# Kernel optimization log

Measured on AMD Instinct MI355X. Metric: run time of the kernel, lower is better.

The kernel has to match this reference:

```python
import jax, jax.numpy as jnp
import numpy as np

NUM_HEADS = 16
D_MODEL = 1024


def setup_inputs() -> dict:
    key = jax.random.key(0)
    ks = jax.random.split(key, 12)
    B, S, D = 2, 2048, D_MODEL
    inp = {
        "query": jax.random.normal(ks[0], (B, S, D), dtype=jnp.float32),
        "key": jax.random.normal(ks[1], (B, S, D), dtype=jnp.float32),
        "value": jax.random.normal(ks[2], (B, S, D), dtype=jnp.float32),
        "mask": jax.random.randint(ks[3], (B, 1, S), 0, 2).astype(jnp.bool_),
    }
    # Linear layer params, stored as (in, out) so y = x @ W + b
    sd = 1.0 / np.sqrt(D)
    for i, nm in enumerate(["q", "k", "v", "o"]):
        inp[f"W{nm}"] = jax.random.uniform(ks[4 + 2 * i], (D, D), jnp.float32, -sd, sd)
        inp[f"b{nm}"] = jax.random.uniform(ks[5 + 2 * i], (D,), jnp.float32, -sd, sd)
    return inp


def _split_heads(x):
    # [B, S, D] -> [B, H, S, d_k]
    B, S, D = x.shape
    return x.reshape(B, S, NUM_HEADS, D // NUM_HEADS).transpose(0, 2, 1, 3)


def reference(query, key, value, mask, Wq, bq, Wk, bk, Wv, bv, Wo, bo):
    B, Sq, D = query.shape
    d_k = D // NUM_HEADS
    scale = 1.0 / np.sqrt(d_k)

    q = _split_heads(query @ Wq + bq)   # [B,H,Sq,dk]
    k = _split_heads(key @ Wk + bk)     # [B,H,Sk,dk]
    v = _split_heads(value @ Wv + bv)   # [B,H,Sk,dk]

    scores = jnp.einsum("bhqd,bhkd->bhqk", q, k) * scale  # [B,H,Sq,Sk]
    # mask: [B,1,Sk] bool, True = masked; broadcast over heads and queries
    scores = jnp.where(mask[:, None, :, :], -jnp.inf, scores)
    attn = jax.nn.softmax(scores, axis=-1)
    attn = jnp.nan_to_num(attn, nan=0.0)  # fully-masked rows -> 0 (matches torch)

    ctx = jnp.einsum("bhqk,bhkd->bhqd", attn, v)  # [B,H,Sq,dk]
    ctx = ctx.transpose(0, 2, 1, 3).reshape(B, Sq, D)  # combine heads
    out = ctx @ Wo + bo
    return out
```

## Files before the change

kernel.cpp:

```cpp
#include <hip/hip_runtime.h>


typedef unsigned short u16;
typedef __attribute__((ext_vector_type(8))) short bf16x8;
typedef __attribute__((ext_vector_type(4))) float f32x4;
typedef __attribute__((ext_vector_type(2))) unsigned int u32x2;

static __device__ __forceinline__ u16 f2bf(float x) {
  union { float f; unsigned int i; } v; v.f = x;
  return (u16)((v.i + 0x8000u) >> 16);
}
static __device__ __forceinline__ float bf2f(u16 u) {
  union { unsigned int i; float f; } v; v.i = ((unsigned int)u) << 16; return v.f;
}

static __device__ __forceinline__ unsigned int cvtpk(float lo, float hi) {
  unsigned int r;
  asm("v_cvt_pk_bf16_f32 %0, %1, %2" : "=v"(r) : "v"(lo), "v"(hi));
  return r;
}

#define MFMA_B16(a, b, c) __builtin_amdgcn_mfma_f32_16x16x32_bf16((a), (b), (c), 0, 0, 0)

__global__ __launch_bounds__(256) void prep_w(
    const float* __restrict__ w0, const float* __restrict__ w1,
    const float* __restrict__ w2, const float* __restrict__ w3,
    u16* __restrict__ t0, u16* __restrict__ t1,
    u16* __restrict__ t2, u16* __restrict__ t3) {
  __shared__ u16 tile[64 * 68];
  const float* W; u16* T;
  switch (blockIdx.z) {
    case 0: W = w0; T = t0; break;
    case 1: W = w1; T = t1; break;
    case 2: W = w2; T = t2; break;
    default: W = w3; T = t3; break;
  }
  const int t = threadIdx.x;
  const int k0 = blockIdx.x * 64, n0 = blockIdx.y * 64;
#pragma unroll
  for (int it = 0; it < 4; ++it) {
    int idx = it * 256 + t;
    int r = idx >> 4, c4 = idx & 15;
    float4 v = *(const float4*)&W[(size_t)(k0 + r) * 1024 + n0 + c4 * 4];
    tile[r * 68 + c4 * 4 + 0] = f2bf(v.x);
    tile[r * 68 + c4 * 4 + 1] = f2bf(v.y);
    tile[r * 68 + c4 * 4 + 2] = f2bf(v.z);
    tile[r * 68 + c4 * 4 + 3] = f2bf(v.w);
  }
  __syncthreads();
#pragma unroll
  for (int it = 0; it < 2; ++it) {
    int idx = it * 256 + t;
    int n = idx >> 3, kc = idx & 7;
    bf16x8 pk;
#pragma unroll
    for (int j = 0; j < 8; ++j) pk[j] = (short)tile[(kc * 8 + j) * 68 + n];
    *(bf16x8*)&T[(size_t)(n0 + n) * 1024 + k0 + kc * 8] = pk;
  }
}

template <int MT, int AMODE, int OMODE>
__global__ __launch_bounds__(256) void gemm_bias(
    const void* a0v, const void* a1v, const void* a2v,
    const u16* __restrict__ Wt,
    const float* b0, const float* b1, const float* b2,
    void* o0, void* o1, void* o2) {
  __shared__ __align__(16) u16 As[MT * 32 * 32];
  __shared__ __align__(16) u16 Bs[128 * 32];
  const int t = threadIdx.x, wave = t >> 6, lane = t & 63;
  const int l15 = lane & 15, quad = lane >> 4;
  const int m0 = blockIdx.x * (MT * 32);
  const int n0 = blockIdx.y * 128;
  const int rg = (OMODE == 3) ? (n0 >> 10) : 0;
  const void* Av = (rg == 0) ? a0v : (rg == 1 ? a1v : a2v);
  const float* bp = (rg == 0) ? b0 : (rg == 1 ? b1 : b2);
  const int nb = (OMODE == 3) ? (n0 & 1023) : n0;
  const int wr = (wave >> 1) * (MT * 16), wc = (wave & 1) * 64;

  const f32x4 fz = {0.f, 0.f, 0.f, 0.f};
  f32x4 acc[MT][4];
#pragma unroll
  for (int mt = 0; mt < MT; ++mt)
#pragma unroll
    for (int nt = 0; nt < 4; ++nt) acc[mt][nt] = fz;

  float4 pa[MT / 2][2]; bf16x8 pab[MT / 2]; bf16x8 pb[2];
#pragma unroll
  for (int s = 0; s < MT / 2; ++s) {
    int idx = s * 256 + t, row = idx >> 2, seg = idx & 3;
    if (AMODE == 1) {
      const float* ap = (const float*)Av + (size_t)(m0 + row) * 1024 + seg * 8;
      pa[s][0] = *(const float4*)ap; pa[s][1] = *(const float4*)(ap + 4);
    } else {
      pab[s] = *(const bf16x8*)((const u16*)Av + (size_t)(m0 + row) * 1024 + seg * 8);
    }
  }
#pragma unroll
  for (int s = 0; s < 2; ++s) {
    int idx = s * 256 + t, row = idx >> 2, seg = idx & 3;
    pb[s] = *(const bf16x8*)&Wt[(size_t)(n0 + row) * 1024 + seg * 8];
  }

  for (int kb = 0; kb < 1024; kb += 32) {
    __syncthreads();
#pragma unroll
    for (int s = 0; s < MT / 2; ++s) {
      int idx = s * 256 + t, row = idx >> 2, seg = idx & 3;
      bf16x8 pk;
      if (AMODE == 1) {
        pk[0] = (short)f2bf(pa[s][0].x); pk[1] = (short)f2bf(pa[s][0].y);
        pk[2] = (short)f2bf(pa[s][0].z); pk[3] = (short)f2bf(pa[s][0].w);
        pk[4] = (short)f2bf(pa[s][1].x); pk[5] = (short)f2bf(pa[s][1].y);
        pk[6] = (short)f2bf(pa[s][1].z); pk[7] = (short)f2bf(pa[s][1].w);
      } else pk = pab[s];
      *(bf16x8*)&As[row * 32 + seg * 8] = pk;
    }
#pragma unroll
    for (int s = 0; s < 2; ++s) {
      int idx = s * 256 + t, row = idx >> 2, seg = idx & 3;
      *(bf16x8*)&Bs[row * 32 + seg * 8] = pb[s];
    }
    __syncthreads();
    const int kn = (kb + 32) & 1023;
#pragma unroll
    for (int s = 0; s < MT / 2; ++s) {
      int idx = s * 256 + t, row = idx >> 2, seg = idx & 3;
      if (AMODE == 1) {
        const float* ap = (const float*)Av + (size_t)(m0 + row) * 1024 + kn + seg * 8;
        pa[s][0] = *(const float4*)ap; pa[s][1] = *(const float4*)(ap + 4);
      } else {
        pab[s] = *(const bf16x8*)((const u16*)Av + (size_t)(m0 + row) * 1024 + kn + seg * 8);
      }
    }
#pragma unroll
    for (int s = 0; s < 2; ++s) {
      int idx = s * 256 + t, row = idx >> 2, seg = idx & 3;
      pb[s] = *(const bf16x8*)&Wt[(size_t)(n0 + row) * 1024 + kn + seg * 8];
    }
    bf16x8 a[MT], bfr[4];
#pragma unroll
    for (int mt = 0; mt < MT; ++mt)
      a[mt] = *(const bf16x8*)&As[(wr + mt * 16 + l15) * 32 + quad * 8];
#pragma unroll
    for (int nt = 0; nt < 4; ++nt)
      bfr[nt] = *(const bf16x8*)&Bs[(wc + nt * 16 + l15) * 32 + quad * 8];
#pragma unroll
    for (int mt = 0; mt < MT; ++mt)
#pragma unroll
      for (int nt = 0; nt < 4; ++nt)
        acc[mt][nt] = MFMA_B16(a[mt], bfr[nt], acc[mt][nt]);
  }

#pragma unroll
  for (int nt = 0; nt < 4; ++nt) {
    const int n = nb + wc + nt * 16 + l15;
    const float bv = bp[n];
#pragma unroll
    for (int mt = 0; mt < MT; ++mt)
#pragma unroll
      for (int r = 0; r < 4; ++r) {
        const int m = m0 + wr + mt * 16 + quad * 4 + r;
        const float val = acc[mt][nt][r] + bv;
        if (OMODE == 2) {
          ((float*)o0)[(size_t)m * 1024 + n] = val;
        } else if (OMODE == 0) {
          ((u16*)o0)[(size_t)m * 1024 + n] = f2bf(val);
        } else {
          if (rg == 0)      ((u16*)o0)[(size_t)m * 1024 + n] = f2bf(val);
          else if (rg == 1) ((u16*)o1)[(size_t)m * 1024 + n] = f2bf(val);
          else {
            const int h = n >> 6, d = n & 63, bb = m >> 11, ss = m & 2047;
            ((u16*)o2)[((size_t)(bb * 16 + h) * 64 + d) * 2048 + ss] = f2bf(val);
          }
        }
      }
  }
}

__global__ __launch_bounds__(512) void attn_fused(
    const u16* Q, const u16* __restrict__ K,
    const u16* __restrict__ Vt, const int* __restrict__ mask,
    u16* ctx) {
  __shared__ __align__(16) u16 Ks[128 * 72];
  __shared__ __align__(16) u16 Vs[64 * 136];
  __shared__ __align__(16) u16 Pl[8][16 * 136];
  __shared__ __align__(16) float Mf[2048];
  const int t = threadIdx.x, wave = t >> 6, lane = t & 63;
  const int l15 = lane & 15, quad = lane >> 4;
  const int bh = blockIdx.y, b = bh >> 4, h = bh & 15;
  const int q0 = blockIdx.x * 128 + wave * 16;
  const float cs = 0.125f * 1.44269504f;

#pragma unroll
  for (int i = 0; i < 4; ++i) {
    int idx = i * 512 + t;
    Mf[idx] = mask[b * 2048 + idx] ? -__builtin_inff() : 0.f;
  }

  const u16* Qp = Q + (size_t)(b * 2048 + q0) * 1024 + h * 64;
  const bf16x8 qf0 = *(const bf16x8*)(Qp + (size_t)l15 * 1024 + quad * 8);
  const bf16x8 qf1 = *(const bf16x8*)(Qp + (size_t)l15 * 1024 + 32 + quad * 8);

  const u16* Kbase = K + (size_t)(b * 2048) * 1024 + h * 64;
  const u16* Vbase = Vt + (size_t)bh * 64 * 2048;

  const int kr0 = t >> 3,        kc0 = (t & 7) * 8;
  const int kr1 = (512 + t) >> 3;
  const int vr0 = t >> 4,        vc0 = (t & 15) * 8;
  const int vr1 = (512 + t) >> 4;

  bf16x8 gk0 = *(const bf16x8*)&Kbase[(size_t)kr0 * 1024 + kc0];
  bf16x8 gk1 = *(const bf16x8*)&Kbase[(size_t)kr1 * 1024 + kc0];
  bf16x8 gv0 = *(const bf16x8*)&Vbase[(size_t)vr0 * 2048 + vc0];
  bf16x8 gv1 = *(const bf16x8*)&Vbase[(size_t)vr1 * 2048 + vc0];

  const f32x4 fz = {0.f, 0.f, 0.f, 0.f};
  f32x4 o[4];
  float lsum = 0.f;
#pragma unroll
  for (int i = 0; i < 4; ++i) o[i] = fz;

  for (int kt = 0; kt < 2048; kt += 128) {
    __syncthreads();
    *(bf16x8*)&Ks[kr0 * 72 + kc0] = gk0;
    *(bf16x8*)&Ks[kr1 * 72 + kc0] = gk1;
    *(bf16x8*)&Vs[vr0 * 136 + vc0] = gv0;
    *(bf16x8*)&Vs[vr1 * 136 + vc0] = gv1;
    __syncthreads();
    const int kn = (kt + 128) & 2047;
    gk0 = *(const bf16x8*)&Kbase[(size_t)(kn + kr0) * 1024 + kc0];
    gk1 = *(const bf16x8*)&Kbase[(size_t)(kn + kr1) * 1024 + kc0];
    gv0 = *(const bf16x8*)&Vbase[(size_t)vr0 * 2048 + kn + vc0];
    gv1 = *(const bf16x8*)&Vbase[(size_t)vr1 * 2048 + kn + vc0];

#pragma unroll
    for (int nt = 0; nt < 8; ++nt) {
      const int krow = nt * 16 + l15;
      bf16x8 k0 = *(const bf16x8*)&Ks[krow * 72 + quad * 8];
      bf16x8 k1 = *(const bf16x8*)&Ks[krow * 72 + 32 + quad * 8];
      f32x4 acc = MFMA_B16(k0, qf0, fz);
      acc = MFMA_B16(k1, qf1, acc);
      const float4 bias4 = *(const float4*)&Mf[kt + nt * 16 + quad * 4];
      float p0 = exp2f(fmaf(acc[0], cs, bias4.x));
      float p1 = exp2f(fmaf(acc[1], cs, bias4.y));
      float p2 = exp2f(fmaf(acc[2], cs, bias4.z));
      float p3 = exp2f(fmaf(acc[3], cs, bias4.w));
      lsum += (p0 + p1) + (p2 + p3);
      u32x2 pp;
      pp.x = cvtpk(p0, p1);
      pp.y = cvtpk(p2, p3);
      *(u32x2*)&Pl[wave][l15 * 136 + nt * 16 + quad * 4] = pp;
    }
#pragma unroll
    for (int kc = 0; kc < 4; ++kc) {
      const bf16x8 pf = *(const bf16x8*)&Pl[wave][l15 * 136 + kc * 32 + quad * 8];
#pragma unroll
      for (int nt = 0; nt < 4; ++nt) {
        const bf16x8 vf = *(const bf16x8*)&Vs[(nt * 16 + l15) * 136 + kc * 32 + quad * 8];
        o[nt] = MFMA_B16(pf, vf, o[nt]);
      }
    }
  }
  lsum += __shfl_xor(lsum, 16);
  lsum += __shfl_xor(lsum, 32);
  u16* cp = ctx + (size_t)(b * 2048 + q0) * 1024 + h * 64;
#pragma unroll
  for (int r = 0; r < 4; ++r) {
    const float lrow = __shfl(lsum, quad * 4 + r);
    const bool ok = lrow > 0.f;
    const float inv = ok ? 1.f / lrow : 0.f;
#pragma unroll
    for (int nt = 0; nt < 4; ++nt)
      cp[(quad * 4 + r) * 1024 + nt * 16 + l15] = f2bf(ok ? o[nt][r] * inv : 0.f);
  }
}

extern "C" void kernel_launch(void* const* d_in, const int* in_sizes, int n_in,
                              void* d_out, int out_size, void* d_ws, size_t ws_size,
                              hipStream_t stream) {
  const float* q    = (const float*)d_in[0];
  const float* k    = (const float*)d_in[1];
  const float* v    = (const float*)d_in[2];
  const int*   mask = (const int*)d_in[3];
  const float* Wq = (const float*)d_in[4];  const float* bq = (const float*)d_in[5];
  const float* Wk = (const float*)d_in[6];  const float* bk = (const float*)d_in[7];
  const float* Wv = (const float*)d_in[8];  const float* bv = (const float*)d_in[9];
  const float* Wo = (const float*)d_in[10]; const float* bo = (const float*)d_in[11];

  char* ws = (char*)d_ws;
  u16*   Kp  = (u16*)(ws + ((size_t)0 << 20));
  u16*   Vt  = (u16*)(ws + ((size_t)8 << 20));
  float* O32 = (float*)ws;

  char* od = (char*)d_out;
  u16* ctx = (u16*)od;
  u16* WqT = (u16*)(od + ((size_t)8 << 20));
  u16* WkT = (u16*)(od + ((size_t)10 << 20));
  u16* WvT = (u16*)(od + ((size_t)12 << 20));
  u16* WoT = (u16*)(od + ((size_t)14 << 20));

  dim3 blk(256);
  prep_w<<<dim3(16, 16, 4), blk, 0, stream>>>(Wq, Wk, Wv, Wo, WqT, WkT, WvT, WoT);
  gemm_bias<4, 1, 3><<<dim3(32, 24), blk, 0, stream>>>(
      q, k, v, WqT, bq, bk, bv, (void*)ctx, (void*)Kp, (void*)Vt);
  attn_fused<<<dim3(16, 32), dim3(512), 0, stream>>>(ctx, Kp, Vt, mask, ctx);
  gemm_bias<2, 0, 2><<<dim3(64, 8), blk, 0, stream>>>(
      ctx, nullptr, nullptr, WoT, bo, nullptr, nullptr, (void*)O32, nullptr, nullptr);
  hipMemcpyAsync(d_out, O32, (size_t)out_size * sizeof(float),
                 hipMemcpyDeviceToDevice, stream);
}
```

Baseline: 263.8 us.

## Swizzle attention LDS tiles, shrink P buffer and stream mask per tile

Replaces padded LDS layouts for K, V and the per-wave P tile with XOR-swizzled unpadded layouts. The P tile is halved by processing the 128-key tile in two 64-key halves. The full 2048-entry mask bias array is replaced by a 128-entry per-tile copy that is prefetched from global memory alongside K/V. LDS use drops substantially, which may allow more resident blocks per CU, and the swizzle aims to avoid bank conflicts. In exchange it adds XOR address arithmetic and a mask load per iteration.

```diff
diff --git a/kernel.cpp b/kernel.cpp
--- a/kernel.cpp
+++ b/kernel.cpp
@@ -9,9 +9,6 @@
 static __device__ __forceinline__ u16 f2bf(float x) {
   union { float f; unsigned int i; } v; v.f = x;
   return (u16)((v.i + 0x8000u) >> 16);
-}
-static __device__ __forceinline__ float bf2f(u16 u) {
-  union { unsigned int i; float f; } v; v.i = ((unsigned int)u) << 16; return v.f;
 }
 
 static __device__ __forceinline__ unsigned int cvtpk(float lo, float hi) {
@@ -181,21 +178,16 @@
     const u16* Q, const u16* __restrict__ K,
     const u16* __restrict__ Vt, const int* __restrict__ mask,
     u16* ctx) {
-  __shared__ __align__(16) u16 Ks[128 * 72];
-  __shared__ __align__(16) u16 Vs[64 * 136];
-  __shared__ __align__(16) u16 Pl[8][16 * 136];
-  __shared__ __align__(16) float Mf[2048];
+  __shared__ __align__(16) u16 Ks[128 * 64];
+  __shared__ __align__(16) u16 Vs[64 * 128];
+  __shared__ __align__(16) u16 Pl[8][16 * 64];
+  __shared__ __align__(16) float Mf[128];
   const int t = threadIdx.x, wave = t >> 6, lane = t & 63;
   const int l15 = lane & 15, quad = lane >> 4;
   const int bh = blockIdx.y, b = bh >> 4, h = bh & 15;
   const int q0 = blockIdx.x * 128 + wave * 16;
   const float cs = 0.125f * 1.44269504f;
-
-#pragma unroll
-  for (int i = 0; i < 4; ++i) {
-    int idx = i * 512 + t;
-    Mf[idx] = mask[b * 2048 + idx] ? -__builtin_inff() : 0.f;
-  }
+  const int swz = (l15 & 7) << 3;
 
   const u16* Qp = Q + (size_t)(b * 2048 + q0) * 1024 + h * 64;
   const bf16x8 qf0 = *(const bf16x8*)(Qp + (size_t)l15 * 1024 + quad * 8);
@@ -204,15 +196,21 @@
   const u16* Kbase = K + (size_t)(b * 2048) * 1024 + h * 64;
   const u16* Vbase = Vt + (size_t)bh * 64 * 2048;
 
-  const int kr0 = t >> 3,        kc0 = (t & 7) * 8;
-  const int kr1 = (512 + t) >> 3;
-  const int vr0 = t >> 4,        vc0 = (t & 15) * 8;
-  const int vr1 = (512 + t) >> 4;
+  const int kr0 = t >> 3,  kc0 = (t & 7) * 8;
+  const int kr1 = 64 + kr0;
+  const int vr0 = t >> 4,  vc0 = (t & 15) * 8;
+  const int vr1 = 32 + vr0;
+  const int ksw0 = (kr0 * 64 + kc0) ^ ((kr0 & 7) << 3);
+  const int ksw1 = (kr1 * 64 + kc0) ^ ((kr0 & 7) << 3);
+  const int vsw0 = (vr0 * 128 + vc0) ^ ((vr0 & 7) << 3);
+  const int vsw1 = (vr1 * 128 + vc0) ^ ((vr1 & 7) << 3);
+  const int mti = t & 127;
 
   bf16x8 gk0 = *(const bf16x8*)&Kbase[(size_t)kr0 * 1024 + kc0];
   bf16x8 gk1 = *(const bf16x8*)&Kbase[(size_t)kr1 * 1024 + kc0];
   bf16x8 gv0 = *(const bf16x8*)&Vbase[(size_t)vr0 * 2048 + vc0];
   bf16x8 gv1 = *(const bf16x8*)&Vbase[(size_t)vr1 * 2048 + vc0];
+  int gm = mask[b * 2048 + mti];
 
   const f32x4 fz = {0.f, 0.f, 0.f, 0.f};
   f32x4 o[4];
@@ -222,42 +220,51 @@
 
   for (int kt = 0; kt < 2048; kt += 128) {
     __syncthreads();
-    *(bf16x8*)&Ks[kr0 * 72 + kc0] = gk0;
-    *(bf16x8*)&Ks[kr1 * 72 + kc0] = gk1;
-    *(bf16x8*)&Vs[vr0 * 136 + vc0] = gv0;
-    *(bf16x8*)&Vs[vr1 * 136 + vc0] = gv1;
+    *(bf16x8*)&Ks[ksw0] = gk0;
+    *(bf16x8*)&Ks[ksw1] = gk1;
+    *(bf16x8*)&Vs[vsw0] = gv0;
+    *(bf16x8*)&Vs[vsw1] = gv1;
+    if (t < 128) Mf[t] = gm ? -__builtin_inff() : 0.f;
     __syncthreads();
     const int kn = (kt + 128) & 2047;
     gk0 = *(const bf16x8*)&Kbase[(size_t)(kn + kr0) * 1024 + kc0];
     gk1 = *(const bf16x8*)&Kbase[(size_t)(kn + kr1) * 1024 + kc0];
     gv0 = *(const bf16x8*)&Vbase[(size_t)vr0 * 2048 + kn + vc0];
     gv1 = *(const bf16x8*)&Vbase[(size_t)vr1 * 2048 + kn + vc0];
-
-#pragma unroll
-    for (int nt = 0; nt < 8; ++nt) {
-      const int krow = nt * 16 + l15;
-      bf16x8 k0 = *(const bf16x8*)&Ks[krow * 72 + quad * 8];
-      bf16x8 k1 = *(const bf16x8*)&Ks[krow * 72 + 32 + quad * 8];
-      f32x4 acc = MFMA_B16(k0, qf0, fz);
-      acc = MFMA_B16(k1, qf1, acc);
-      const float4 bias4 = *(const float4*)&Mf[kt + nt * 16 + quad * 4];
-      float p0 = exp2f(fmaf(acc[0], cs, bias4.x));
-      float p1 = exp2f(fmaf(acc[1], cs, bias4.y));
-      float p2 = exp2f(fmaf(acc[2], cs, bias4.z));
-      float p3 = exp2f(fmaf(acc[3], cs, bias4.w));
-      lsum += (p0 + p1) + (p2 + p3);
-      u32x2 pp;
-      pp.x = cvtpk(p0, p1);
-      pp.y = cvtpk(p2, p3);
-      *(u32x2*)&Pl[wave][l15 * 136 + nt * 16 + quad * 4] = pp;
-    }
-#pragma unroll
-    for (int kc = 0; kc < 4; ++kc) {
-      const bf16x8 pf = *(const bf16x8*)&Pl[wave][l15 * 136 + kc * 32 + quad * 8];
+    gm  = mask[b * 2048 + kn + mti];
+
+#pragma unroll
+    for (int h2 = 0; h2 < 2; ++h2) {
 #pragma unroll
       for (int nt = 0; nt < 4; ++nt) {
-        const bf16x8 vf = *(const bf16x8*)&Vs[(nt * 16 + l15) * 136 + kc * 32 + quad * 8];
-        o[nt] = MFMA_B16(pf, vf, o[nt]);
+        const int g = h2 * 4 + nt;
+        const int krow = g * 16 + l15;
+        bf16x8 k0 = *(const bf16x8*)&Ks[(krow * 64 + quad * 8) ^ swz];
+        bf16x8 k1 = *(const bf16x8*)&Ks[(krow * 64 + 32 + quad * 8) ^ swz];
+        f32x4 acc = MFMA_B16(k0, qf0, fz);
+        acc = MFMA_B16(k1, qf1, acc);
+        const float4 bias4 = *(const float4*)&Mf[g * 16 + quad * 4];
+        float p0 = exp2f(fmaf(acc[0], cs, bias4.x));
+        float p1 = exp2f(fmaf(acc[1], cs, bias4.y));
+        float p2 = exp2f(fmaf(acc[2], cs, bias4.z));
+        float p3 = exp2f(fmaf(acc[3], cs, bias4.w));
+        lsum += (p0 + p1) + (p2 + p3);
+        u32x2 pp;
+        pp.x = cvtpk(p0, p1);
+        pp.y = cvtpk(p2, p3);
+        *(u32x2*)&Pl[wave][(l15 * 64 + nt * 16 + quad * 4) ^ swz] = pp;
+      }
+#pragma unroll
+      for (int kcc = 0; kcc < 2; ++kcc) {
+        const int kc = h2 * 2 + kcc;
+        const bf16x8 pf =
+            *(const bf16x8*)&Pl[wave][(l15 * 64 + kcc * 32 + quad * 8) ^ swz];
+#pragma unroll
+        for (int nt = 0; nt < 4; ++nt) {
+          const bf16x8 vf = *(const bf16x8*)
+              &Vs[((nt * 16 + l15) * 128 + kc * 32 + quad * 8) ^ swz];
+          o[nt] = MFMA_B16(pf, vf, o[nt]);
+        }
       }
     }
   }
```

Measured after the change: 261.0 us. Within noise of the previous version (-1.1%).

## Rewrite attention kernel with 32x32 MFMA, register-resident P and ballot masks

Applied to the files above, without the earlier changes.

Moves the attention kernel from 16x16x32 to 32x32x16 bf16 MFMA, with 4 waves of 32 query rows each instead of 8 waves of 16. Probabilities are passed from the QK^T accumulator straight into the PV operand through permlane32_swap, which removes the per-wave LDS round trip for P. The mask is read per tile, turned into a bitmask with ballot and applied by bit-masking exp results, replacing the shared float bias array. K and V tiles use XOR-swizzled LDS layouts to avoid bank conflicts. The costs are higher register pressure and fewer waves per block.

```diff
diff --git a/kernel.cpp b/kernel.cpp
--- a/kernel.cpp
+++ b/kernel.cpp
@@ -2,25 +2,25 @@
 
 
 typedef unsigned short u16;
+typedef unsigned int u32;
 typedef __attribute__((ext_vector_type(8))) short bf16x8;
 typedef __attribute__((ext_vector_type(4))) float f32x4;
-typedef __attribute__((ext_vector_type(2))) unsigned int u32x2;
+typedef __attribute__((ext_vector_type(16))) float f32x16;
+typedef __attribute__((ext_vector_type(2))) int i32x2;
 
 static __device__ __forceinline__ u16 f2bf(float x) {
-  union { float f; unsigned int i; } v; v.f = x;
+  union { float f; u32 i; } v; v.f = x;
   return (u16)((v.i + 0x8000u) >> 16);
 }
-static __device__ __forceinline__ float bf2f(u16 u) {
-  union { unsigned int i; float f; } v; v.i = ((unsigned int)u) << 16; return v.f;
-}
-
-static __device__ __forceinline__ unsigned int cvtpk(float lo, float hi) {
-  unsigned int r;
+
+static __device__ __forceinline__ u32 cvtpk(float lo, float hi) {
+  u32 r;
   asm("v_cvt_pk_bf16_f32 %0, %1, %2" : "=v"(r) : "v"(lo), "v"(hi));
   return r;
 }
 
 #define MFMA_B16(a, b, c) __builtin_amdgcn_mfma_f32_16x16x32_bf16((a), (b), (c), 0, 0, 0)
+#define MFMA32_B16(a, b, c) __builtin_amdgcn_mfma_f32_32x32x16_bf16((a), (b), (c), 0, 0, 0)
 
 __global__ __launch_bounds__(256) void prep_w(
     const float* __restrict__ w0, const float* __restrict__ w1,
@@ -177,101 +177,137 @@
   }
 }
 
-__global__ __launch_bounds__(512) void attn_fused(
+__global__ __launch_bounds__(256) void attn_fused(
     const u16* Q, const u16* __restrict__ K,
     const u16* __restrict__ Vt, const int* __restrict__ mask,
     u16* ctx) {
-  __shared__ __align__(16) u16 Ks[128 * 72];
-  __shared__ __align__(16) u16 Vs[64 * 136];
-  __shared__ __align__(16) u16 Pl[8][16 * 136];
-  __shared__ __align__(16) float Mf[2048];
+  __shared__ __align__(16) u16 Ks[8 * 128 * 8];
+  __shared__ __align__(16) u16 Vs[16 * 64 * 8];
+  __shared__ float Lw[4][32];
   const int t = threadIdx.x, wave = t >> 6, lane = t & 63;
-  const int l15 = lane & 15, quad = lane >> 4;
+  const int l31 = lane & 31, hi = lane >> 5;
   const int bh = blockIdx.y, b = bh >> 4, h = bh & 15;
-  const int q0 = blockIdx.x * 128 + wave * 16;
+  const int q0w = blockIdx.x * 128 + wave * 32;
   const float cs = 0.125f * 1.44269504f;
 
-#pragma unroll
-  for (int i = 0; i < 4; ++i) {
-    int idx = i * 512 + t;
-    Mf[idx] = mask[b * 2048 + idx] ? -__builtin_inff() : 0.f;
-  }
-
-  const u16* Qp = Q + (size_t)(b * 2048 + q0) * 1024 + h * 64;
-  const bf16x8 qf0 = *(const bf16x8*)(Qp + (size_t)l15 * 1024 + quad * 8);
-  const bf16x8 qf1 = *(const bf16x8*)(Qp + (size_t)l15 * 1024 + 32 + quad * 8);
+  const u16* Qp2 = Q + (size_t)(b * 2048 + q0w) * 1024 + h * 64;
+  bf16x8 qb[4];
+#pragma unroll
+  for (int kd = 0; kd < 4; ++kd)
+    qb[kd] = *(const bf16x8*)(Qp2 + (size_t)l31 * 1024 + kd * 16 + hi * 8);
 
   const u16* Kbase = K + (size_t)(b * 2048) * 1024 + h * 64;
   const u16* Vbase = Vt + (size_t)bh * 64 * 2048;
 
-  const int kr0 = t >> 3,        kc0 = (t & 7) * 8;
-  const int kr1 = (512 + t) >> 3;
-  const int vr0 = t >> 4,        vc0 = (t & 15) * 8;
-  const int vr1 = (512 + t) >> 4;
-
-  bf16x8 gk0 = *(const bf16x8*)&Kbase[(size_t)kr0 * 1024 + kc0];
-  bf16x8 gk1 = *(const bf16x8*)&Kbase[(size_t)kr1 * 1024 + kc0];
-  bf16x8 gv0 = *(const bf16x8*)&Vbase[(size_t)vr0 * 2048 + vc0];
-  bf16x8 gv1 = *(const bf16x8*)&Vbase[(size_t)vr1 * 2048 + vc0];
-
-  const f32x4 fz = {0.f, 0.f, 0.f, 0.f};
-  f32x4 o[4];
+  bf16x8 gk[4], gv[4];
+#pragma unroll
+  for (int s = 0; s < 4; ++s) {
+    int slot = s * 256 + t;
+    int kr = slot >> 3, ksg = slot & 7;
+    gk[s] = *(const bf16x8*)&Kbase[(size_t)kr * 1024 + ksg * 8];
+    int vr = slot >> 4, vsg = slot & 15;
+    gv[s] = *(const bf16x8*)&Vbase[(size_t)vr * 2048 + vsg * 8];
+  }
+  int mk0 = mask[b * 2048 + lane];
+  int mk1 = mask[b * 2048 + 64 + lane];
+
+  const f32x16 sz = {0.f};
+  f32x16 o0a = sz, o1a = sz;
   float lsum = 0.f;
-#pragma unroll
-  for (int i = 0; i < 4; ++i) o[i] = fz;
+  const int hs = hi * 4;
 
   for (int kt = 0; kt < 2048; kt += 128) {
     __syncthreads();
-    *(bf16x8*)&Ks[kr0 * 72 + kc0] = gk0;
-    *(bf16x8*)&Ks[kr1 * 72 + kc0] = gk1;
-    *(bf16x8*)&Vs[vr0 * 136 + vc0] = gv0;
-    *(bf16x8*)&Vs[vr1 * 136 + vc0] = gv1;
+#pragma unroll
+    for (int s = 0; s < 4; ++s) {
+      int slot = s * 256 + t;
+      int kr = slot >> 3, ksg = slot & 7;
+      *(bf16x8*)&Ks[ksg * 1024 + ((kr ^ (ksg & 7)) * 8)] = gk[s];
+      int vr = slot >> 4, vsg = slot & 15;
+      *(bf16x8*)&Vs[vsg * 512 + ((vr ^ (vsg & 7)) * 8)] = gv[s];
+    }
+    const unsigned long long mb0 = __ballot(mk0 == 0);
+    const unsigned long long mb1 = __ballot(mk1 == 0);
+    const u32 mw[4] = {(u32)mb0, (u32)(mb0 >> 32), (u32)mb1, (u32)(mb1 >> 32)};
     __syncthreads();
     const int kn = (kt + 128) & 2047;
-    gk0 = *(const bf16x8*)&Kbase[(size_t)(kn + kr0) * 1024 + kc0];
-    gk1 = *(const bf16x8*)&Kbase[(size_t)(kn + kr1) * 1024 + kc0];
-    gv0 = *(const bf16x8*)&Vbase[(size_t)vr0 * 2048 + kn + vc0];
-    gv1 = *(const bf16x8*)&Vbase[(size_t)vr1 * 2048 + kn + vc0];
-
-#pragma unroll
-    for (int nt = 0; nt < 8; ++nt) {
-      const int krow = nt * 16 + l15;
-      bf16x8 k0 = *(const bf16x8*)&Ks[krow * 72 + quad * 8];
-      bf16x8 k1 = *(const bf16x8*)&Ks[krow * 72 + 32 + quad * 8];
-      f32x4 acc = MFMA_B16(k0, qf0, fz);
-      acc = MFMA_B16(k1, qf1, acc);
-      const float4 bias4 = *(const float4*)&Mf[kt + nt * 16 + quad * 4];
-      float p0 = exp2f(fmaf(acc[0], cs, bias4.x));
-      float p1 = exp2f(fmaf(acc[1], cs, bias4.y));
-      float p2 = exp2f(fmaf(acc[2], cs, bias4.z));
-      float p3 = exp2f(fmaf(acc[3], cs, bias4.w));
-      lsum += (p0 + p1) + (p2 + p3);
-      u32x2 pp;
-      pp.x = cvtpk(p0, p1);
-      pp.y = cvtpk(p2, p3);
-      *(u32x2*)&Pl[wave][l15 * 136 + nt * 16 + quad * 4] = pp;
-    }
-#pragma unroll
-    for (int kc = 0; kc < 4; ++kc) {
-      const bf16x8 pf = *(const bf16x8*)&Pl[wave][l15 * 136 + kc * 32 + quad * 8];
-#pragma unroll
-      for (int nt = 0; nt < 4; ++nt) {
-        const bf16x8 vf = *(const bf16x8*)&Vs[(nt * 16 + l15) * 136 + kc * 32 + quad * 8];
-        o[nt] = MFMA_B16(pf, vf, o[nt]);
-      }
-    }
-  }
-  lsum += __shfl_xor(lsum, 16);
+#pragma unroll
+    for (int s = 0; s < 4; ++s) {
+      int slot = s * 256 + t;
+      int kr = slot >> 3, ksg = slot & 7;
+      gk[s] = *(const bf16x8*)&Kbase[(size_t)(kn + kr) * 1024 + ksg * 8];
+      int vr = slot >> 4, vsg = slot & 15;
+      gv[s] = *(const bf16x8*)&Vbase[(size_t)vr * 2048 + kn + vsg * 8];
+    }
+    mk0 = mask[b * 2048 + kn + lane];
+    mk1 = mask[b * 2048 + kn + 64 + lane];
+
+#pragma unroll
+    for (int kg = 0; kg < 4; ++kg) {
+      f32x16 S = sz;
+#pragma unroll
+      for (int kd = 0; kd < 4; ++kd) {
+        const int dseg = kd * 2 + hi;
+        const bf16x8 kf = *(const bf16x8*)
+            &Ks[dseg * 1024 + (((kg * 32 + l31) ^ (dseg & 7)) * 8)];
+        S = MFMA32_B16(kf, qb[kd], S);
+      }
+      const u32 mws = mw[kg] >> hs;
+      u32 W[8];
+      float p[16];
+#pragma unroll
+      for (int c = 0; c < 4; ++c) {
+#pragma unroll
+        for (int j = 0; j < 4; ++j) {
+          float pv = exp2f(S[c * 4 + j] * cs);
+          pv = __int_as_float(__float_as_int(pv) &
+                              (-(int)((mws >> (8 * c + j)) & 1u)));
+          p[c * 4 + j] = pv;
+          lsum += pv;
+        }
+        W[2 * c + 0] = cvtpk(p[c * 4 + 0], p[c * 4 + 1]);
+        W[2 * c + 1] = cvtpk(p[c * 4 + 2], p[c * 4 + 3]);
+      }
+      {
+        i32x2 r0 = __builtin_amdgcn_permlane32_swap((int)W[0], (int)W[2], false, false);
+        i32x2 r1 = __builtin_amdgcn_permlane32_swap((int)W[1], (int)W[3], false, false);
+        i32x2 r2 = __builtin_amdgcn_permlane32_swap((int)W[4], (int)W[6], false, false);
+        i32x2 r3 = __builtin_amdgcn_permlane32_swap((int)W[5], (int)W[7], false, false);
+        union { bf16x8 v; u32 w[4]; } pa0, pa1;
+        pa0.w[0] = (u32)r0[0]; pa0.w[1] = (u32)r1[0];
+        pa0.w[2] = (u32)r0[1]; pa0.w[3] = (u32)r1[1];
+        pa1.w[0] = (u32)r2[0]; pa1.w[1] = (u32)r3[0];
+        pa1.w[2] = (u32)r2[1]; pa1.w[3] = (u32)r3[1];
+#pragma unroll
+        for (int ks2 = 0; ks2 < 2; ++ks2) {
+          const bf16x8 pav = ks2 ? pa1.v : pa0.v;
+          const int kseg = (kg * 2 + ks2) * 2 + hi;
+          const bf16x8 vf0 = *(const bf16x8*)
+              &Vs[kseg * 512 + ((l31 ^ (kseg & 7)) * 8)];
+          const bf16x8 vf1 = *(const bf16x8*)
+              &Vs[kseg * 512 + (((32 + l31) ^ (kseg & 7)) * 8)];
+          o0a = MFMA32_B16(pav, vf0, o0a);
+          o1a = MFMA32_B16(pav, vf1, o1a);
+        }
+      }
+    }
+  }
   lsum += __shfl_xor(lsum, 32);
-  u16* cp = ctx + (size_t)(b * 2048 + q0) * 1024 + h * 64;
-#pragma unroll
-  for (int r = 0; r < 4; ++r) {
-    const float lrow = __shfl(lsum, quad * 4 + r);
-    const bool ok = lrow > 0.f;
-    const float inv = ok ? 1.f / lrow : 0.f;
-#pragma unroll
-    for (int nt = 0; nt < 4; ++nt)
-      cp[(quad * 4 + r) * 1024 + nt * 16 + l15] = f2bf(ok ? o[nt][r] * inv : 0.f);
+  {
+    const float inv = lsum > 0.f ? 1.f / lsum : 0.f;
+    if (hi == 0) Lw[wave][l31] = inv;
+  }
+  u16* cp = ctx + (size_t)(b * 2048 + q0w) * 1024 + h * 64;
+#pragma unroll
+  for (int c = 0; c < 4; ++c) {
+    const float4 iv4 = *(const float4*)&Lw[wave][c * 8 + hi * 4];
+#pragma unroll
+    for (int j = 0; j < 4; ++j) {
+      const int row = 8 * c + 4 * hi + j;
+      const float iv = (&iv4.x)[j];
+      cp[(size_t)row * 1024 + l31]      = f2bf(o0a[c * 4 + j] * iv);
+      cp[(size_t)row * 1024 + 32 + l31] = f2bf(o1a[c * 4 + j] * iv);
+    }
   }
 }
 
@@ -303,7 +339,7 @@
   prep_w<<<dim3(16, 16, 4), blk, 0, stream>>>(Wq, Wk, Wv, Wo, WqT, WkT, WvT, WoT);
   gemm_bias<4, 1, 3><<<dim3(32, 24), blk, 0, stream>>>(
       q, k, v, WqT, bq, bk, bv, (void*)ctx, (void*)Kp, (void*)Vt);
-  attn_fused<<<dim3(16, 32), dim3(512), 0, stream>>>(ctx, Kp, Vt, mask, ctx);
+  attn_fused<<<dim3(16, 32), dim3(256), 0, stream>>>(ctx, Kp, Vt, mask, ctx);
   gemm_bias<2, 0, 2><<<dim3(64, 8), blk, 0, stream>>>(
       ctx, nullptr, nullptr, WoT, bo, nullptr, nullptr, (void*)O32, nullptr, nullptr);
   hipMemcpyAsync(d_out, O32, (size_t)out_size * sizeof(float),
```

Measured after the change: 265.0 us. About the same (+0.5%).
